# Kernel tuning notes

Hardware: AMD Instinct MI355X
Metric: run time of the kernel (lower is better)

The kernel has to match this reference:

```python
import jax, jax.numpy as jnp
import numpy as np


def setup_inputs() -> dict:
    key = jax.random.key(0)
    kx, kd = jax.random.split(key)
    B, T, D = 16, 1024, 512
    x = jax.random.normal(kx, (B, T, D), dtype=jnp.float32)
    durations = jax.random.randint(kd, (B, T), 0, 8, dtype=jnp.int64)
    return {"x": x, "durations": durations, "max_len": 4096}


def reference(x, durations, max_len):
    # x: [B,T,D], durations: [B,T] int, max_len: static int
    B, T, D = x.shape
    dur = jnp.maximum(durations.astype(jnp.int32), 0)          # clamp(min=0)
    csum = jnp.cumsum(dur, axis=1)                              # [B,T] inclusive cumsum
    total = csum[:, -1]                                         # [B] total frames per row
    pos = jnp.arange(max_len, dtype=jnp.int32)                  # [L] output frame indices
    # source token for output frame j: first t with csum[t] > j (== repeat_interleave)
    src = jax.vmap(lambda c: jnp.searchsorted(c, pos, side='right'))(csum)  # [B,L]
    src = jnp.minimum(src, T - 1)                               # clamp for out-of-range frames
    out = jnp.take_along_axis(x, src[..., None], axis=1)        # [B,L,D] single parallel gather
    mask = pos[None, :] < total[:, None]                        # [B,L] valid frames
    return jnp.where(mask[..., None], out, jnp.zeros((), x.dtype))
```

## Files before the change

### kernel.cpp

```cpp
#include <hip/hip_runtime.h>


#define BB 16
#define TT 1024
#define DD 512
#define MAXLEN 4096

__global__ __launch_bounds__(256) void build_src_kernel(
    const int* __restrict__ dur, int* __restrict__ srcTab) {
  const int b = blockIdx.x;
  const int tid = threadIdx.x;

  __shared__ int lds[256];
  __shared__ int s_total;

  const int t0 = tid * 4;
  const int* dp = dur + b * TT + t0;
  int d0 = max(dp[0], 0);
  int d1 = max(dp[1], 0);
  int d2 = max(dp[2], 0);
  int d3 = max(dp[3], 0);
  const int s1 = d0 + d1;
  const int s2 = s1 + d2;
  const int s3 = s2 + d3;

  lds[tid] = s3;
  __syncthreads();

  int val = s3;
  for (int off = 1; off < 256; off <<= 1) {
    int other = (tid >= off) ? lds[tid - off] : 0;
    __syncthreads();
    val += other;
    lds[tid] = val;
    __syncthreads();
  }
  const int incl = val;
  const int excl = incl - s3;

  if (tid == 255) s_total = incl;
  __syncthreads();
  const int total = s_total;

  int c[4] = {excl + d0, excl + s1, excl + s2, excl + s3};
  int dd4[4] = {d0, d1, d2, d3};
  int* st = srcTab + b * MAXLEN;
#pragma unroll
  for (int j = 0; j < 4; ++j) {
    const int end = c[j];
    for (int p = end - dd4[j]; p < end; ++p) st[p] = t0 + j;
  }
  for (int p = total + tid; p < MAXLEN; p += 256) st[p] = -1;
}

__global__ __launch_bounds__(256) void gather_kernel(
    const float4* __restrict__ x, const int* __restrict__ srcTab,
    float4* __restrict__ out) {
  const int wave = (int)((blockIdx.x * 256u + threadIdx.x) >> 6);
  const int lane = threadIdx.x & 63;
  const int row = wave;
  const int b = row >> 12;
  const int src = srcTab[row];

  float4* op = out + (size_t)row * (DD / 4);
  if (src < 0) {
    const float4 z = {0.f, 0.f, 0.f, 0.f};
    op[lane] = z;
    op[lane + 64] = z;
  } else {
    const float4* ip = x + ((size_t)b * TT + (size_t)src) * (DD / 4);
    op[lane] = ip[lane];
    op[lane + 64] = ip[lane + 64];
  }
}

extern "C" void kernel_launch(void* const* d_in, const int* in_sizes, int n_in,
                              void* d_out, int out_size, void* d_ws,
                              size_t ws_size, hipStream_t stream) {
  const float* x = (const float*)d_in[0];
  const int* dur = (const int*)d_in[1];
  int* srcTab = (int*)d_ws;

  build_src_kernel<<<BB, 256, 0, stream>>>(dur, srcTab);

  const int rows = BB * MAXLEN;
  gather_kernel<<<rows / 4, 256, 0, stream>>>((const float4*)x, srcTab,
                                              (float4*)d_out);
}
```

Measured before the change: 159.8 us.

## Use wave-shuffle scan for source table and batch four rows per wave with nontemporal stores

```diff
diff --git a/kernel.cpp b/kernel.cpp
--- a/kernel.cpp
+++ b/kernel.cpp
@@ -6,71 +6,72 @@
 #define DD 512
 #define MAXLEN 4096
 
-__global__ __launch_bounds__(256) void build_src_kernel(
+typedef float v4f __attribute__((ext_vector_type(4)));
+
+__global__ __launch_bounds__(1024) void build_src_kernel(
     const int* __restrict__ dur, int* __restrict__ srcTab) {
   const int b = blockIdx.x;
   const int tid = threadIdx.x;
+  const int lane = tid & 63;
+  const int wid = tid >> 6;
 
-  __shared__ int lds[256];
+  const int d = max(dur[b * TT + tid], 0);
+
+  int v = d;
+#pragma unroll
+  for (int off = 1; off < 64; off <<= 1) {
+    int n = __shfl_up(v, off, 64);
+    if (lane >= off) v += n;
+  }
+
+  __shared__ int wsum[16];
   __shared__ int s_total;
-
-  const int t0 = tid * 4;
-  const int* dp = dur + b * TT + t0;
-  int d0 = max(dp[0], 0);
-  int d1 = max(dp[1], 0);
-  int d2 = max(dp[2], 0);
-  int d3 = max(dp[3], 0);
-  const int s1 = d0 + d1;
-  const int s2 = s1 + d2;
-  const int s3 = s2 + d3;
-
-  lds[tid] = s3;
+  if (lane == 63) wsum[wid] = v;
   __syncthreads();
 
-  int val = s3;
-  for (int off = 1; off < 256; off <<= 1) {
-    int other = (tid >= off) ? lds[tid - off] : 0;
-    __syncthreads();
-    val += other;
-    lds[tid] = val;
-    __syncthreads();
-  }
-  const int incl = val;
-  const int excl = incl - s3;
+  int add = 0;
+  for (int i = 0; i < wid; ++i) add += wsum[i];
+  const int incl = v + add;
+  const int excl = incl - d;
 
-  if (tid == 255) s_total = incl;
+  if (tid == TT - 1) s_total = incl;
   __syncthreads();
   const int total = s_total;
 
-  int c[4] = {excl + d0, excl + s1, excl + s2, excl + s3};
-  int dd4[4] = {d0, d1, d2, d3};
   int* st = srcTab + b * MAXLEN;
-#pragma unroll
-  for (int j = 0; j < 4; ++j) {
-    const int end = c[j];
-    for (int p = end - dd4[j]; p < end; ++p) st[p] = t0 + j;
-  }
-  for (int p = total + tid; p < MAXLEN; p += 256) st[p] = -1;
+  for (int p = excl; p < incl; ++p) st[p] = tid;
+  for (int p = total + tid; p < MAXLEN; p += 1024) st[p] = -1;
 }
 
 __global__ __launch_bounds__(256) void gather_kernel(
-    const float4* __restrict__ x, const int* __restrict__ srcTab,
-    float4* __restrict__ out) {
-  const int wave = (int)((blockIdx.x * 256u + threadIdx.x) >> 6);
+    const v4f* __restrict__ x, const int* __restrict__ srcTab,
+    v4f* __restrict__ out) {
+  const int gw = (int)(blockIdx.x * 4u + (threadIdx.x >> 6));
   const int lane = threadIdx.x & 63;
-  const int row = wave;
-  const int b = row >> 12;
-  const int src = srcTab[row];
+  const int base = gw * 4;
+  const int b = base >> 12;
 
-  float4* op = out + (size_t)row * (DD / 4);
-  if (src < 0) {
-    const float4 z = {0.f, 0.f, 0.f, 0.f};
-    op[lane] = z;
-    op[lane + 64] = z;
-  } else {
-    const float4* ip = x + ((size_t)b * TT + (size_t)src) * (DD / 4);
-    op[lane] = ip[lane];
-    op[lane + 64] = ip[lane + 64];
+  int s[4];
+#pragma unroll
+  for (int i = 0; i < 4; ++i) s[i] = srcTab[base + i];
+
+  v4f v0[4], v1[4];
+  const v4f* xb = x + (size_t)b * TT * (DD / 4);
+#pragma unroll
+  for (int i = 0; i < 4; ++i) {
+    const int src = (s[i] < 0) ? 0 : s[i];
+    const v4f* ip = xb + (size_t)src * (DD / 4);
+    v0[i] = ip[lane];
+    v1[i] = ip[lane + 64];
+  }
+
+  const v4f z = {0.f, 0.f, 0.f, 0.f};
+#pragma unroll
+  for (int i = 0; i < 4; ++i) {
+    if (s[i] < 0) { v0[i] = z; v1[i] = z; }
+    v4f* op = out + (size_t)(base + i) * (DD / 4);
+    __builtin_nontemporal_store(v0[i], op + lane);
+    __builtin_nontemporal_store(v1[i], op + lane + 64);
   }
 }
 
@@ -81,9 +82,9 @@
   const int* dur = (const int*)d_in[1];
   int* srcTab = (int*)d_ws;
 
-  build_src_kernel<<<BB, 256, 0, stream>>>(dur, srcTab);
+  build_src_kernel<<<BB, 1024, 0, stream>>>(dur, srcTab);
 
   const int rows = BB * MAXLEN;
-  gather_kernel<<<rows / 4, 256, 0, stream>>>((const float4*)x, srcTab,
-                                              (float4*)d_out);
+  gather_kernel<<<rows / 16, 256, 0, stream>>>((const v4f*)x, srcTab,
+                                               (v4f*)d_out);
 }
```

Measured after the change: 168.1 us. +5.2%, slower.
